# Performance work log

Measured on AMD Instinct MI355X. Metric: run time of the kernel, lower is better.

## Reference

```python
import jax, jax.numpy as jnp
import numpy as np

N, M, D, DV = 8192, 8192, 512, 512

def setup_inputs() -> dict:
    key = jax.random.key(0)
    kq, kk, kv = jax.random.split(key, 3)
    return {
        "query": jax.random.normal(kq, (N, D), dtype=jnp.float32),
        "key": jax.random.normal(kk, (M, D), dtype=jnp.float32),
        "value": jax.random.normal(kv, (M, DV), dtype=jnp.float32),
    }

def reference(query, key, value):
    # scores: [N, M] = Q @ K^T (no scale, no mask, matching the torch module)
    scores = query @ key.T
    attn = jax.nn.softmax(scores, axis=-1)
    return attn @ value
```

## Files before the change

### kernel.cpp

```cpp
#include <hip/hip_runtime.h>
#include <hip/hip_fp16.h>
#include <stdint.h>

typedef _Float16 f16;
typedef _Float16 f16x8 __attribute__((ext_vector_type(8)));
typedef float    f32x4 __attribute__((ext_vector_type(4)));
typedef int      i32x4 __attribute__((ext_vector_type(4)));

#define NQ 8192
#define NK 8192
#define DD 512
#define DVV 512
#define LOG2E 1.44269504f
#define KT256 (NK / 256)

__device__ __forceinline__ void stage16(const void* g, void* ldsbase, int lane) {
#if __has_builtin(__builtin_amdgcn_global_load_lds)
  __builtin_amdgcn_global_load_lds((const __attribute__((address_space(1))) void*)g,
                                   (__attribute__((address_space(3))) void*)ldsbase, 16, 0, 0);
#else
  ((i32x4*)ldsbase)[lane] = *(const i32x4*)g;
#endif
}

__global__ void conv_f16k(const float* __restrict__ src, f16* __restrict__ dst, int n8) {
  int i = blockIdx.x * 256 + threadIdx.x;
  if (i >= n8) return;
  const float4* s4 = (const float4*)src;
  float4 a = s4[2 * i], b = s4[2 * i + 1];
  float vv[8] = {a.x, a.y, a.z, a.w, b.x, b.y, b.z, b.w};
  f16 h8[8];
#pragma unroll
  for (int j = 0; j < 8; ++j) h8[j] = (f16)vv[j];
  *(f16x8*)(dst + (size_t)i * 8) = *(f16x8*)h8;
}

__global__ void conv_vT(const float* __restrict__ v, f16* __restrict__ vT) {
  __shared__ float t[64][65];
  int k0 = blockIdx.x * 64, d0 = blockIdx.y * 64;
#pragma unroll
  for (int e = 0; e < 16; ++e) {
    int idx = threadIdx.x + e * 256;
    int kr = idx >> 6, dc = idx & 63;
    t[kr][dc] = v[(size_t)(k0 + kr) * DVV + d0 + dc];
  }
  __syncthreads();
  int dl = threadIdx.x >> 2, seg = (threadIdx.x & 3) * 16;
  f16 tmp[16];
#pragma unroll
  for (int c = 0; c < 16; ++c) tmp[c] = (f16)t[seg + c][dl];
  f16* dst = vT + (size_t)(d0 + dl) * NK + k0 + seg;
  *(f16x8*)dst = *(f16x8*)tmp;
  *(f16x8*)(dst + 8) = *(f16x8*)(tmp + 8);
}

__global__ __launch_bounds__(512, 2) void qk_kernel(
    const f16* __restrict__ q16, const f16* __restrict__ k16,
    f16* __restrict__ s16, float* __restrict__ pmT, float* __restrict__ psT,
    int nrows) {
  __shared__ f16 LS[65536];
  __shared__ float red[2][4][128];
  const int tid = threadIdx.x, lane = tid & 63, wid = tid >> 6;
  const int wr = wid >> 2, wc = wid & 3;
  const int bx = blockIdx.x, by = blockIdx.y;
  const int lo16 = lane & 15, hi4 = lane >> 4;

  f32x4 acc[8][4] = {};

  const int srw = lane >> 3, sc8 = (lane & 7) ^ srw;
  const f16* aptr[4]; const f16* bptr[4]; int adst[4], bdst[4];
#pragma unroll
  for (int u = 0; u < 4; ++u) {
    int r = wid * 32 + u * 8 + srw;
    aptr[u] = q16 + (size_t)(by * 256 + r) * DD + sc8 * 8;
    bptr[u] = k16 + (size_t)(bx * 256 + r) * DD + sc8 * 8;
    adst[u] = (wid * 32 + u * 8) * 64;
    bdst[u] = adst[u] + 16384;
  }
  int aoff[8][2], boff[4][2];
#pragma unroll
  for (int m = 0; m < 8; ++m)
#pragma unroll
    for (int kk = 0; kk < 2; ++kk) {
      int row = wr * 128 + m * 16 + lo16;
      aoff[m][kk] = row * 64 + (((kk * 4 + hi4) ^ (row & 7)) << 3);
    }
#pragma unroll
  for (int n = 0; n < 4; ++n)
#pragma unroll
    for (int kk = 0; kk < 2; ++kk) {
      int row = wc * 64 + n * 16 + lo16;
      boff[n][kk] = 16384 + row * 64 + (((kk * 4 + hi4) ^ (row & 7)) << 3);
    }

#define STG(t2, buf)                                                        \
  do {                                                                      \
    _Pragma("unroll") for (int u = 0; u < 4; ++u) {                         \
      stage16(aptr[u] + (t2) * 64, LS + (buf) * 32768 + adst[u], lane);     \
      stage16(bptr[u] + (t2) * 64, LS + (buf) * 32768 + bdst[u], lane);     \
    }                                                                       \
  } while (0)

  STG(0, 0);
  asm volatile("s_waitcnt vmcnt(0)" ::: "memory");
  __builtin_amdgcn_s_barrier();
  asm volatile("" ::: "memory");

  for (int t = 0; t < 8; ++t) {
    const int cur = t & 1;
    if (t < 7) STG(t + 1, cur ^ 1);
    const f16* Bb = LS + cur * 32768;
    f16x8 bf[2][4];
#pragma unroll
    for (int n = 0; n < 4; ++n)
#pragma unroll
      for (int kk = 0; kk < 2; ++kk) bf[kk][n] = *(const f16x8*)&Bb[boff[n][kk]];
#pragma unroll
    for (int h = 0; h < 2; ++h) {
      f16x8 af[4][2];
#pragma unroll
      for (int mi = 0; mi < 4; ++mi)
#pragma unroll
        for (int kk = 0; kk < 2; ++kk) af[mi][kk] = *(const f16x8*)&Bb[aoff[h * 4 + mi][kk]];
      __builtin_amdgcn_s_setprio(1);
#pragma unroll
      for (int mi = 0; mi < 4; ++mi)
#pragma unroll
        for (int n = 0; n < 4; ++n) {
          acc[h * 4 + mi][n] =
              __builtin_amdgcn_mfma_f32_16x16x32_f16(af[mi][0], bf[0][n], acc[h * 4 + mi][n], 0, 0, 0);
          acc[h * 4 + mi][n] =
              __builtin_amdgcn_mfma_f32_16x16x32_f16(af[mi][1], bf[1][n], acc[h * 4 + mi][n], 0, 0, 0);
        }
      __builtin_amdgcn_s_setprio(0);
    }
    asm volatile("s_waitcnt vmcnt(0)" ::: "memory");
    __builtin_amdgcn_s_barrier();
    asm volatile("" ::: "memory");
  }
#undef STG

  float rmax[8][4];
#pragma unroll
  for (int i = 0; i < 8; ++i)
#pragma unroll
    for (int r = 0; r < 4; ++r) {
      float m = fmaxf(fmaxf(acc[i][0][r], acc[i][1][r]), fmaxf(acc[i][2][r], acc[i][3][r]));
#pragma unroll
      for (int d = 1; d < 16; d <<= 1) m = fmaxf(m, __shfl_xor(m, d, 64));
      rmax[i][r] = m;
    }
  if (lo16 == 0) {
#pragma unroll
    for (int i = 0; i < 8; ++i)
#pragma unroll
      for (int r = 0; r < 4; ++r) red[wr][wc][i * 16 + hi4 * 4 + r] = rmax[i][r];
  }
  __syncthreads();
  float pmv[8][4];
#pragma unroll
  for (int i = 0; i < 8; ++i)
#pragma unroll
    for (int r = 0; r < 4; ++r) {
      int rl = i * 16 + hi4 * 4 + r;
      pmv[i][r] = fmaxf(fmaxf(red[wr][0][rl], red[wr][1][rl]),
                        fmaxf(red[wr][2][rl], red[wr][3][rl]));
    }
  __syncthreads();
  float rsum[8][4];
#pragma unroll
  for (int i = 0; i < 8; ++i)
#pragma unroll
    for (int r = 0; r < 4; ++r) {
      int qloc = wr * 128 + i * 16 + hi4 * 4 + r;
      int swz = (qloc & 7) << 3;
      float s = 0.f;
#pragma unroll
      for (int j = 0; j < 4; ++j) {
        float p = exp2f((acc[i][j][r] - pmv[i][r]) * LOG2E);
        s += p;
        int kloc = wc * 64 + j * 16 + lo16;
        LS[qloc * 256 + ((kloc & ~7) ^ swz) + (kloc & 7)] = (f16)p;
      }
#pragma unroll
      for (int d = 1; d < 16; d <<= 1) s += __shfl_xor(s, d, 64);
      rsum[i][r] = s;
    }
  if (lo16 == 0) {
#pragma unroll
    for (int i = 0; i < 8; ++i)
#pragma unroll
      for (int r = 0; r < 4; ++r) red[wr][wc][i * 16 + hi4 * 4 + r] = rsum[i][r];
  }
  __syncthreads();
  if (wc == 0 && lo16 == 0) {
#pragma unroll
    for (int i = 0; i < 8; ++i)
#pragma unroll
      for (int r = 0; r < 4; ++r) {
        int rl = i * 16 + hi4 * 4 + r;
        size_t grow = (size_t)(by * 256 + wr * 128 + rl);
        pmT[(size_t)bx * nrows + grow] = pmv[i][r];
        psT[(size_t)bx * nrows + grow] = red[wr][0][rl] + red[wr][1][rl] +
                                         red[wr][2][rl] + red[wr][3][rl];
      }
  }
  {
    const int q = tid >> 1, half = tid & 1;
    const int swz = (q & 7) << 3;
    f16* gdst = s16 + ((size_t)(by * KT256 + bx) << 16) + q * 256 + half * 128;
#pragma unroll
    for (int e = 0; e < 16; ++e) {
      int k0 = half * 128 + e * 8;
      f16x8 v = *(const f16x8*)&LS[q * 256 + (k0 ^ swz)];
      *(f16x8*)(gdst + e * 8) = v;
    }
  }
}

__global__ void red_kernel(const float* __restrict__ pmT, const float* __restrict__ psT,
                           float* __restrict__ coefT, int nrows) {
  int row = blockIdx.x * 8 + (threadIdx.x >> 5);
  int t = threadIdx.x & 31;
  float pmt = pmT[(size_t)t * nrows + row];
  float m = pmt;
#pragma unroll
  for (int d = 1; d < 32; d <<= 1) m = fmaxf(m, __shfl_xor(m, d, 32));
  float e = exp2f((pmt - m) * LOG2E);
  float l = psT[(size_t)t * nrows + row] * e;
#pragma unroll
  for (int d = 1; d < 32; d <<= 1) l += __shfl_xor(l, d, 32);
  coefT[(size_t)t * nrows + row] = e / l;
}

__global__ __launch_bounds__(256, 2) void pv_kernel(
    const f16* __restrict__ p16, const float* __restrict__ coefT,
    const f16* __restrict__ vT, float* __restrict__ dst,
    int steps, size_t zstride, int nrows) {
  __shared__ f16 lsA[2][128 * 64];
  __shared__ f16 lsB[2][128 * 64];
  const int tid = threadIdx.x, lane = tid & 63, wid = tid >> 6;
  const int lo16 = lane & 15, hi4 = lane >> 4;
  const int wr = wid >> 1, wc = wid & 1;
  const int bx = blockIdx.x, by = blockIdx.y, bz = blockIdx.z;
  const int g0 = bz * steps;
  f32x4 acc[4][4] = {};

  const int arow0 = tid >> 3, acol = tid & 7;
  const int srw = lane >> 3;
  const int sc = (lane & 7) ^ srw;

  size_t qtb[4];
#pragma unroll
  for (int u = 0; u < 4; ++u) {
    int r = by * 128 + u * 32 + arow0;
    qtb[u] = ((size_t)(r >> 8) * KT256 << 16) + (size_t)(r & 255) * 256 + acol * 8;
  }

  f16x8 va[4];
  float scv[4];

#define PV_LOADA(g)                                                           \
  do {                                                                        \
    _Pragma("unroll") for (int u = 0; u < 4; ++u)                             \
        va[u] = *(const f16x8*)(p16 + qtb[u] + ((size_t)((g) >> 2) << 16) +   \
                                ((g) & 3) * 64);                              \
    _Pragma("unroll") for (int u = 0; u < 4; ++u)                             \
        scv[u] = coefT[(size_t)((g) >> 2) * nrows + by * 128 + u * 32 + arow0]; \
  } while (0)

  PV_LOADA(g0);
#pragma unroll
  for (int i = 0; i < 4; ++i) {
    int unit = wid * 4 + i;
    int row = unit * 8 + srw;
    stage16(vT + (size_t)(bx * 128 + row) * NK + (size_t)g0 * 64 + sc * 8,
            &lsB[0][unit * 512], lane);
  }
#pragma unroll
  for (int u = 0; u < 4; ++u) {
    int row = u * 32 + arow0;
    f16x8 vv = va[u] * (f16)scv[u];
    *(f16x8*)&lsA[0][row * 64 + ((acol ^ (row & 7)) << 3)] = vv;
  }
  __syncthreads();

  for (int s = 0; s < steps; ++s) {
    const int cur = s & 1, nxt = cur ^ 1;
    const int g = g0 + s;
    if (s + 1 < steps) {
      PV_LOADA(g + 1);
#pragma unroll
      for (int i = 0; i < 4; ++i) {
        int unit = wid * 4 + i;
        int row = unit * 8 + srw;
        stage16(vT + (size_t)(bx * 128 + row) * NK + (size_t)(g + 1) * 64 + sc * 8,
                &lsB[nxt][unit * 512], lane);
      }
    }
#pragma unroll
    for (int ks = 0; ks < 2; ++ks) {
      f16x8 af[4], bf[4];
#pragma unroll
      for (int i = 0; i < 4; ++i) {
        int row = wr * 64 + i * 16 + lo16;
        af[i] = *(const f16x8*)&lsA[cur][row * 64 + (((ks * 4 + hi4) ^ (row & 7)) << 3)];
      }
#pragma unroll
      for (int j = 0; j < 4; ++j) {
        int dv = wc * 64 + j * 16 + lo16;
        bf[j] = *(const f16x8*)&lsB[cur][dv * 64 + (((ks * 4 + hi4) ^ (dv & 7)) << 3)];
      }
#pragma unroll
      for (int i = 0; i < 4; ++i)
#pragma unroll
        for (int j = 0; j < 4; ++j)
          acc[i][j] = __builtin_amdgcn_mfma_f32_16x16x32_f16(af[i], bf[j], acc[i][j], 0, 0, 0);
    }
    if (s + 1 < steps) {
#pragma unroll
      for (int u = 0; u < 4; ++u) {
        int row = u * 32 + arow0;
        f16x8 vv = va[u] * (f16)scv[u];
        *(f16x8*)&lsA[nxt][row * 64 + ((acol ^ (row & 7)) << 3)] = vv;
      }
    }
    __syncthreads();
  }
#undef PV_LOADA

  float* o = dst + (size_t)bz * zstride;
#pragma unroll
  for (int i = 0; i < 4; ++i)
#pragma unroll
    for (int j = 0; j < 4; ++j)
#pragma unroll
      for (int r = 0; r < 4; ++r)
        o[(size_t)(by * 128 + wr * 64 + i * 16 + hi4 * 4 + r) * DVV +
          bx * 128 + wc * 64 + j * 16 + lo16] = acc[i][j][r];
}

__global__ void reduce_out(const float* __restrict__ part, float* __restrict__ out,
                           int ks, size_t n4) {
  size_t i = (size_t)blockIdx.x * 256 + threadIdx.x;
  if (i >= n4) return;
  float4 a = ((const float4*)part)[i];
  for (int z = 1; z < ks; ++z) {
    float4 b = ((const float4*)(part + z * n4 * 4))[i];
    a.x += b.x; a.y += b.y; a.z += b.z; a.w += b.w;
  }
  ((float4*)out)[i] = a;
}

__global__ void zero_out(float* o, int n) {
  int i = blockIdx.x * 256 + threadIdx.x;
  if (i < n) o[i] = 0.f;
}

extern "C" void kernel_launch(void* const* d_in, const int* in_sizes, int n_in,
                              void* d_out, int out_size, void* d_ws, size_t ws_size,
                              hipStream_t stream) {
  (void)in_sizes; (void)n_in; (void)out_size;
  const float* Q = (const float*)d_in[0];
  const float* K = (const float*)d_in[1];
  const float* V = (const float*)d_in[2];
  float* out = (float*)d_out;

  const size_t sz16 = (size_t)NK * DD * 2;
  const size_t fixedB = 2 * sz16;
  const size_t perRow = 1024 + 32 * 4 * 3 + (size_t)NK * 2;
  const size_t partB = (size_t)16384 * DVV * 4;
  int nc = 0;
  for (int cand = 8192; cand >= 1024; cand >>= 1)
    if (fixedB + (size_t)cand * perRow + partB <= ws_size) { nc = cand; break; }
  if (nc == 0) {
    zero_out<<<(NQ * DVV + 255) / 256, 256, 0, stream>>>(out, NQ * DVV);
    return;
  }
  const int ks = 16384 / nc;
  const int steps = 128 / ks;

  char* w = (char*)d_ws;
  f16* k16 = (f16*)w;
  f16* vT = (f16*)(w + sz16);
  char* p = w + fixedB;
  f16* q16 = (f16*)p;       p += (size_t)nc * 1024;
  float* pmT = (float*)p;   p += (size_t)nc * 128;
  float* psT = (float*)p;   p += (size_t)nc * 128;
  float* coefT = (float*)p; p += (size_t)nc * 128;
  f16* s16 = (f16*)p;       p += (size_t)nc * NK * 2;
  float* part = (float*)p;

  conv_f16k<<<NK * DD / 8 / 256, 256, 0, stream>>>(K, k16, NK * DD / 8);
  conv_vT<<<dim3(NK / 64, DVV / 64), 256, 0, stream>>>(V, vT);

  for (int c = 0; c < NQ / nc; ++c) {
    conv_f16k<<<nc * DD / 8 / 256, 256, 0, stream>>>(Q + (size_t)c * nc * DD, q16, nc * DD / 8);
    qk_kernel<<<dim3(NK / 256, nc / 256), 512, 0, stream>>>(q16, k16, s16, pmT, psT, nc);
    red_kernel<<<nc / 8, 256, 0, stream>>>(pmT, psT, coefT, nc);
    pv_kernel<<<dim3(DVV / 128, nc / 128, ks), 256, 0, stream>>>(
        s16, coefT, vT, part, steps, (size_t)nc * DVV, nc);
    reduce_out<<<(int)(((size_t)nc * DVV / 4 + 255) / 256), 256, 0, stream>>>(
        part, out + (size_t)c * nc * DVV, ks, (size_t)nc * DVV / 4);
  }
}
```

Baseline: 265.1 us.

## Split QK^T K-step into four barrier-fenced phases with explicit LDS waits

Result: no change. 268.5 us (+1.3%).

```diff
diff --git a/kernel.cpp b/kernel.cpp
--- a/kernel.cpp
+++ b/kernel.cpp
@@ -93,7 +93,7 @@
       boff[n][kk] = 16384 + row * 64 + (((kk * 4 + hi4) ^ (row & 7)) << 3);
     }
 
-#define STG(t2, buf)                                                        \
+#define STG8(t2, buf)                                                       \
   do {                                                                      \
     _Pragma("unroll") for (int u = 0; u < 4; ++u) {                         \
       stage16(aptr[u] + (t2) * 64, LS + (buf) * 32768 + adst[u], lane);     \
@@ -101,44 +101,76 @@
     }                                                                       \
   } while (0)
 
-  STG(0, 0);
+#define MFMA16(hh, kk)                                                      \
+  do {                                                                      \
+    __builtin_amdgcn_s_setprio(1);                                          \
+    _Pragma("unroll") for (int mi = 0; mi < 4; ++mi)                        \
+    _Pragma("unroll") for (int n = 0; n < 4; ++n)                           \
+        acc[(hh) * 4 + mi][n] = __builtin_amdgcn_mfma_f32_16x16x32_f16(     \
+            af[mi], bf[n], acc[(hh) * 4 + mi][n], 0, 0, 0);                 \
+    __builtin_amdgcn_s_setprio(0);                                          \
+    (void)(kk);                                                             \
+  } while (0)
+
+#define BAR()                                                               \
+  do {                                                                      \
+    asm volatile("" ::: "memory");                                          \
+    __builtin_amdgcn_s_barrier();                                           \
+    asm volatile("" ::: "memory");                                          \
+  } while (0)
+
+  STG8(0, 0);
   asm volatile("s_waitcnt vmcnt(0)" ::: "memory");
-  __builtin_amdgcn_s_barrier();
-  asm volatile("" ::: "memory");
+  BAR();
 
   for (int t = 0; t < 8; ++t) {
     const int cur = t & 1;
-    if (t < 7) STG(t + 1, cur ^ 1);
     const f16* Bb = LS + cur * 32768;
-    f16x8 bf[2][4];
-#pragma unroll
-    for (int n = 0; n < 4; ++n)
-#pragma unroll
-      for (int kk = 0; kk < 2; ++kk) bf[kk][n] = *(const f16x8*)&Bb[boff[n][kk]];
-#pragma unroll
-    for (int h = 0; h < 2; ++h) {
-      f16x8 af[4][2];
-#pragma unroll
-      for (int mi = 0; mi < 4; ++mi)
-#pragma unroll
-        for (int kk = 0; kk < 2; ++kk) af[mi][kk] = *(const f16x8*)&Bb[aoff[h * 4 + mi][kk]];
-      __builtin_amdgcn_s_setprio(1);
-#pragma unroll
-      for (int mi = 0; mi < 4; ++mi)
-#pragma unroll
-        for (int n = 0; n < 4; ++n) {
-          acc[h * 4 + mi][n] =
-              __builtin_amdgcn_mfma_f32_16x16x32_f16(af[mi][0], bf[0][n], acc[h * 4 + mi][n], 0, 0, 0);
-          acc[h * 4 + mi][n] =
-              __builtin_amdgcn_mfma_f32_16x16x32_f16(af[mi][1], bf[1][n], acc[h * 4 + mi][n], 0, 0, 0);
-        }
-      __builtin_amdgcn_s_setprio(0);
-    }
+    f16x8 af[4], bf[4];
+
+#pragma unroll
+    for (int n = 0; n < 4; ++n) bf[n] = *(const f16x8*)&Bb[boff[n][0]];
+#pragma unroll
+    for (int mi = 0; mi < 4; ++mi) af[mi] = *(const f16x8*)&Bb[aoff[mi][0]];
+    if (t < 7) STG8(t + 1, cur ^ 1);
+    BAR();
+    asm volatile("s_waitcnt lgkmcnt(0)" ::: "memory");
+    __builtin_amdgcn_sched_barrier(0);
+    MFMA16(0, 0);
+    BAR();
+
+#pragma unroll
+    for (int mi = 0; mi < 4; ++mi) af[mi] = *(const f16x8*)&Bb[aoff[4 + mi][0]];
+    BAR();
+    asm volatile("s_waitcnt lgkmcnt(0)" ::: "memory");
+    __builtin_amdgcn_sched_barrier(0);
+    MFMA16(1, 0);
+    BAR();
+
+#pragma unroll
+    for (int n = 0; n < 4; ++n) bf[n] = *(const f16x8*)&Bb[boff[n][1]];
+#pragma unroll
+    for (int mi = 0; mi < 4; ++mi) af[mi] = *(const f16x8*)&Bb[aoff[mi][1]];
+    BAR();
+    asm volatile("s_waitcnt lgkmcnt(0)" ::: "memory");
+    __builtin_amdgcn_sched_barrier(0);
+    MFMA16(0, 1);
+    BAR();
+
+#pragma unroll
+    for (int mi = 0; mi < 4; ++mi) af[mi] = *(const f16x8*)&Bb[aoff[4 + mi][1]];
+    BAR();
+    asm volatile("s_waitcnt lgkmcnt(0)" ::: "memory");
+    __builtin_amdgcn_sched_barrier(0);
+    MFMA16(1, 1);
     asm volatile("s_waitcnt vmcnt(0)" ::: "memory");
-    __builtin_amdgcn_s_barrier();
-    asm volatile("" ::: "memory");
-  }
-#undef STG
+    BAR();
+  }
+#undef STG8
+#undef MFMA16
+#undef BAR
+
+  __syncthreads();
 
   float rmax[8][4];
 #pragma unroll
```
